# Kernel optimization log

Hardware: AMD Instinct MI355X
Metric: run time of the kernel (lower is better)

Reference implementation:

```python
import jax, jax.numpy as jnp
import numpy as np

N = 100000      # nodes
E = 3200000     # edges
F_IN = 256      # in_channels
H = 64          # hidden_channels
C = 2           # out_channels
G = 128         # graphs in batch


def setup_inputs() -> dict:
    key = jax.random.key(0)
    ks = jax.random.split(key, 10)
    x = jax.random.normal(ks[0], (N, F_IN), jnp.float32)
    edge_index = jax.random.randint(ks[1], (2, E), 0, N, dtype=jnp.int64)
    batch = jnp.sort(jax.random.randint(ks[2], (N,), 0, G, dtype=jnp.int64))
    s = 0.05
    W1 = jax.random.normal(ks[3], (F_IN, H), jnp.float32) * s
    b1 = jnp.zeros((H,), jnp.float32)
    W2 = jax.random.normal(ks[4], (H, H), jnp.float32) * s
    b2 = jnp.zeros((H,), jnp.float32)
    fc_W = jax.random.normal(ks[5], (H, C), jnp.float32) * s
    fc_b = jnp.zeros((C,), jnp.float32)
    return {"x": x, "edge_index": edge_index, "batch": batch,
            "W1": W1, "b1": b1, "W2": W2, "b2": b2,
            "fc_W": fc_W, "fc_b": fc_b}


def _gcn_layer(h, src, dst, norm, W, b, n_nodes):
    # PyG GCNConv: linear transform first, then normalized aggregate, then bias
    h = h @ W                                   # [N, H]
    msg = h[src] * norm[:, None]                # [E+N, H] gather + scale
    out = jax.ops.segment_sum(msg, dst, num_segments=n_nodes)
    return out + b


def reference(x, edge_index, batch, W1, b1, W2, b2, fc_W, fc_b):
    n_nodes = x.shape[0]
    # add self loops (GCNConv default)
    loop = jnp.arange(n_nodes, dtype=edge_index.dtype)
    src = jnp.concatenate([edge_index[0], loop])
    dst = jnp.concatenate([edge_index[1], loop])
    # symmetric normalization D^{-1/2} (A+I) D^{-1/2}
    deg = jax.ops.segment_sum(jnp.ones_like(src, dtype=x.dtype), dst,
                              num_segments=n_nodes)
    deg_isqrt = jnp.where(deg > 0, jax.lax.rsqrt(deg), 0.0)
    norm = deg_isqrt[src] * deg_isqrt[dst]

    h = jax.nn.relu(_gcn_layer(x, src, dst, norm, W1, b1, n_nodes))
    h = jax.nn.relu(_gcn_layer(h, src, dst, norm, W2, b2, n_nodes))

    # global mean pool over graphs
    n_graphs = G
    sums = jax.ops.segment_sum(h, batch, num_segments=n_graphs)
    cnts = jax.ops.segment_sum(jnp.ones((n_nodes,), h.dtype), batch,
                               num_segments=n_graphs)
    pooled = sums / jnp.clip(cnts, 1.0)[:, None]  # [G, H]
    return pooled @ fc_W + fc_b                   # [G, C]
```

## Files before the change

kernel.cpp:

```cpp
#include <hip/hip_runtime.h>
#include <hip/hip_bf16.h>


#define F_IN 256
#define HDIM 64
#define BR_SHIFT 7
#define BRANGE 128
#define BCAP 4608
#define CHUNK 8192
#define NBK 788

typedef short short8 __attribute__((ext_vector_type(8)));
typedef short short4v __attribute__((ext_vector_type(4)));
typedef float float4v __attribute__((ext_vector_type(4)));
typedef _Float16 half_t;

__device__ __forceinline__ unsigned bf16_rn(float f) {
  unsigned u = __builtin_bit_cast(unsigned, f);
  return (u + 0x7FFFu + ((u >> 16) & 1u)) >> 16;
}
__device__ __forceinline__ float bf16_to_f32(unsigned h) {
  return __builtin_bit_cast(float, h << 16);
}

__global__ __launch_bounds__(256) void bin_kernel(
    const int* __restrict__ src, const int* __restrict__ dst,
    int* __restrict__ gcur, int* __restrict__ entries, int E, int nb) {
  __shared__ int out32[CHUNK];
  __shared__ int pref[NBK + 1];
  __shared__ int cur[NBK];
  __shared__ int gbase[NBK];
  __shared__ int sscan[256];
  const int tid = threadIdx.x;
  for (int i = tid; i < nb; i += 256) cur[i] = 0;
  __syncthreads();
  long e0 = (long)blockIdx.x * CHUNK;
  int cnt = (int)min((long)CHUNK, (long)E - e0);
  for (int i = tid; i < cnt; i += 256)
    atomicAdd(&cur[dst[e0 + i] >> BR_SHIFT], 1);
  __syncthreads();
  int b0 = tid * 4;
  int h[4];
  int s = 0;
#pragma unroll
  for (int i = 0; i < 4; ++i) {
    h[i] = (b0 + i < nb) ? cur[b0 + i] : 0;
    s += h[i];
  }
  int x = s;
  sscan[tid] = x;
  __syncthreads();
  for (int off = 1; off < 256; off <<= 1) {
    int t = (tid >= off) ? sscan[tid - off] : 0;
    __syncthreads();
    sscan[tid] += t;
    __syncthreads();
  }
  int run = sscan[tid] - x;
#pragma unroll
  for (int i = 0; i < 4; ++i) {
    if (b0 + i < nb) {
      pref[b0 + i] = run;
      cur[b0 + i] = run;
      if (h[i] > 0) gbase[b0 + i] = atomicAdd(&gcur[b0 + i], h[i]);
      run += h[i];
    }
  }
  if (tid == 0) pref[nb] = cnt;
  __syncthreads();
  for (int i = tid; i < cnt; i += 256) {
    int d = dst[e0 + i];
    int sv = src[e0 + i];
    int b = d >> BR_SHIFT;
    int r = atomicAdd(&cur[b], 1);
    out32[r] = ((d & (BRANGE - 1)) << 17) | sv;
  }
  __syncthreads();
  for (int j = tid; j < cnt; j += 256) {
    int lo = 0, hi = nb - 1;
    while (lo < hi) {
      int mid = (lo + hi + 1) >> 1;
      if (pref[mid] <= j) lo = mid; else hi = mid - 1;
    }
    int b = lo;
    int slot = gbase[b] + (j - pref[b]);
    if (slot < BCAP) entries[(size_t)b * BCAP + slot] = out32[j];
  }
}

__global__ __launch_bounds__(256) void bucket_scan_kernel(
    const int* __restrict__ gcur, int* __restrict__ bbase,
    int* __restrict__ rowptr, int nb, int N, int E) {
  __shared__ int sscan[256];
  const int tid = threadIdx.x;
  int b0 = tid * 4;
  int h[4];
  int s = 0;
#pragma unroll
  for (int i = 0; i < 4; ++i) {
    h[i] = (b0 + i < nb) ? min(gcur[b0 + i], BCAP) : 0;
    s += h[i];
  }
  int x = s;
  sscan[tid] = x;
  __syncthreads();
  for (int off = 1; off < 256; off <<= 1) {
    int t = (tid >= off) ? sscan[tid - off] : 0;
    __syncthreads();
    sscan[tid] += t;
    __syncthreads();
  }
  int run = sscan[tid] - x;
#pragma unroll
  for (int i = 0; i < 4; ++i) {
    if (b0 + i < nb) {
      bbase[b0 + i] = run;
      run += h[i];
    }
  }
  if (tid == 0) rowptr[N] = E;
}

__global__ __launch_bounds__(256) void csr_build_kernel(
    const int* __restrict__ entries, const int* __restrict__ gcur,
    const int* __restrict__ bbase, int* __restrict__ rowptr,
    float* __restrict__ dnorm, int* __restrict__ csr, int N) {
  __shared__ int lbuf[BCAP];
  __shared__ int lcnt[BRANGE];
  __shared__ int lpref[BRANGE];
  __shared__ int lcur[BRANGE];
  const int b = blockIdx.x, tid = threadIdx.x;
  const int v0 = b * BRANGE;
  const int nloc = min(BRANGE, N - v0);
  if (tid < BRANGE) lcnt[tid] = 0;
  __syncthreads();
  const int cnt = min(gcur[b], BCAP);
  const int base = bbase[b];
  const int* ep = entries + (size_t)b * BCAP;
  for (int i = tid; i < cnt; i += 256) atomicAdd(&lcnt[ep[i] >> 17], 1);
  __syncthreads();
  if (tid < BRANGE) lpref[tid] = lcnt[tid];
  __syncthreads();
  for (int off = 1; off < BRANGE; off <<= 1) {
    int t = 0;
    if (tid < BRANGE && tid >= off) t = lpref[tid - off];
    __syncthreads();
    if (tid < BRANGE) lpref[tid] += t;
    __syncthreads();
  }
  if (tid < BRANGE) {
    int excl = lpref[tid] - lcnt[tid];
    lcur[tid] = excl;
    if (tid < nloc) {
      rowptr[v0 + tid] = base + excl;
      dnorm[v0 + tid] = rsqrtf((float)lcnt[tid] + 1.0f);
    }
  }
  __syncthreads();
  for (int i = tid; i < cnt; i += 256) {
    int e = ep[i];
    int dl = e >> 17;
    int pos = atomicAdd(&lcur[dl], 1);
    if (pos < BCAP) lbuf[pos] = e & 0x1FFFF;
  }
  __syncthreads();
  int* outp = csr + base;
  for (int i = tid; i < cnt; i += 256) outp[i] = lbuf[i];
}

template <int K>
__global__ __launch_bounds__(256) void wfrag_kernel(
    const float* __restrict__ W, short* __restrict__ whi,
    short* __restrict__ wlo) {
  constexpr int KS = K / 32;
  int slot = blockIdx.x * 256 + threadIdx.x;
  if (slot >= 4 * KS * 64 * 8) return;
  int j = slot & 7;
  int lane = (slot >> 3) & 63;
  int fk = slot >> 9;
  int ks = fk % KS;
  int ct = fk / KS;
  int k = ks * 32 + (lane >> 4) * 8 + j;
  int n = ct * 16 + (lane & 15);
  float w = W[k * 64 + n];
  unsigned h = bf16_rn(w);
  unsigned l = bf16_rn(w - bf16_to_f32(h));
  whi[slot] = (short)h;
  wlo[slot] = (short)l;
}

template <int K, typename OT>
__global__ __launch_bounds__(512) void mfma_gemm_kernel(
    const float* __restrict__ X, const short* __restrict__ whi,
    const short* __restrict__ wlo, const float* __restrict__ dnorm,
    OT* __restrict__ out, int N) {
  constexpr int KS = K / 32;
  constexpr int P = K + 8;
  __shared__ __align__(16) short Ahi[64 * P];
  __shared__ __align__(16) short Alo[64 * P];
  const int tid = threadIdx.x;
  const long base = (long)blockIdx.x * 64;
  constexpr int C4 = K / 4;
  constexpr int NL = 64 * C4 / 512;
#pragma unroll
  for (int i = 0; i < NL; ++i) {
    int idx = tid + i * 512;
    int row = idx / C4;
    int c4 = idx % C4;
    long r = base + row;
    if (r >= N) r = N - 1;
    float4v v = *(const float4v*)&X[(size_t)r * K + c4 * 4];
    short4v hv, lv;
#pragma unroll
    for (int j = 0; j < 4; ++j) {
      float f = v[j];
      unsigned h = bf16_rn(f);
      unsigned l = bf16_rn(f - bf16_to_f32(h));
      hv[j] = (short)h;
      lv[j] = (short)l;
    }
    *(short4v*)&Ahi[row * P + c4 * 4] = hv;
    *(short4v*)&Alo[row * P + c4 * 4] = lv;
  }
  __syncthreads();
  const int lane = tid & 63;
  const int wave = tid >> 6;
  const int rt = wave & 3;
  const int chalf = wave >> 2;
  const int m = lane & 15;
  const int q = lane >> 4;
  const int arow = rt * 16 + m;
  float4v acc[2];
  acc[0] = (float4v){0.f, 0.f, 0.f, 0.f};
  acc[1] = (float4v){0.f, 0.f, 0.f, 0.f};
  for (int ks = 0; ks < KS; ++ks) {
    int koff = ks * 32 + q * 8;
    short8 ah = *(const short8*)&Ahi[arow * P + koff];
    short8 al = *(const short8*)&Alo[arow * P + koff];
#pragma unroll
    for (int cc = 0; cc < 2; ++cc) {
      int ct = chalf * 2 + cc;
      size_t fo = ((size_t)(ct * KS + ks) * 64 + lane) * 8;
      short8 bh = *(const short8*)&whi[fo];
      short8 bl = *(const short8*)&wlo[fo];
      acc[cc] = __builtin_amdgcn_mfma_f32_16x16x32_bf16(ah, bh, acc[cc], 0, 0, 0);
      acc[cc] = __builtin_amdgcn_mfma_f32_16x16x32_bf16(ah, bl, acc[cc], 0, 0, 0);
      acc[cc] = __builtin_amdgcn_mfma_f32_16x16x32_bf16(al, bh, acc[cc], 0, 0, 0);
    }
  }
#pragma unroll
  for (int reg = 0; reg < 4; ++reg) {
    long grow = base + rt * 16 + q * 4 + reg;
    if (grow < N) {
      float dn = dnorm[grow];
#pragma unroll
      for (int cc = 0; cc < 2; ++cc) {
        int ct = chalf * 2 + cc;
        out[grow * 64 + ct * 16 + m] = (OT)(acc[cc][reg] * dn);
      }
    }
  }
}

__global__ __launch_bounds__(256) void gather_agg_kernel(
    const half_t* __restrict__ hs, const int* __restrict__ rowptr,
    const int* __restrict__ csr, const float* __restrict__ dnorm,
    const float* __restrict__ bias, float* __restrict__ hout, int N) {
  const int lane = threadIdx.x & 63;
  const int wave = __builtin_amdgcn_readfirstlane((int)(threadIdx.x >> 6));
  int v = blockIdx.x * 4 + wave;
  if (v >= N) return;
  int beg = rowptr[v], end = rowptr[v + 1];
  float a0 = (float)hs[(size_t)v * 64 + lane];
  float a1 = 0.f, a2 = 0.f, a3 = 0.f, a4 = 0.f, a5 = 0.f, a6 = 0.f, a7 = 0.f;
  int j = beg;
  for (; j + 8 <= end; j += 8) {
    int s0 = csr[j], s1 = csr[j + 1], s2 = csr[j + 2], s3 = csr[j + 3];
    int s4 = csr[j + 4], s5 = csr[j + 5], s6 = csr[j + 6], s7 = csr[j + 7];
    a0 += (float)hs[(size_t)s0 * 64 + lane];
    a1 += (float)hs[(size_t)s1 * 64 + lane];
    a2 += (float)hs[(size_t)s2 * 64 + lane];
    a3 += (float)hs[(size_t)s3 * 64 + lane];
    a4 += (float)hs[(size_t)s4 * 64 + lane];
    a5 += (float)hs[(size_t)s5 * 64 + lane];
    a6 += (float)hs[(size_t)s6 * 64 + lane];
    a7 += (float)hs[(size_t)s7 * 64 + lane];
  }
  for (; j + 4 <= end; j += 4) {
    int s0 = csr[j], s1 = csr[j + 1], s2 = csr[j + 2], s3 = csr[j + 3];
    a0 += (float)hs[(size_t)s0 * 64 + lane];
    a1 += (float)hs[(size_t)s1 * 64 + lane];
    a2 += (float)hs[(size_t)s2 * 64 + lane];
    a3 += (float)hs[(size_t)s3 * 64 + lane];
  }
  for (; j < end; ++j) a0 += (float)hs[(size_t)csr[j] * 64 + lane];
  float val = dnorm[v] * (((a0 + a1) + (a2 + a3)) + ((a4 + a5) + (a6 + a7))) +
              bias[lane];
  hout[(size_t)v * 64 + lane] = fmaxf(val, 0.f);
}

__global__ __launch_bounds__(256) void gather_agg_pool_kernel(
    const half_t* __restrict__ hs, const int* __restrict__ rowptr,
    const int* __restrict__ csr, const float* __restrict__ dnorm,
    const float* __restrict__ bias, const int* __restrict__ batch,
    float* __restrict__ pooled, int N) {
  const int lane = threadIdx.x & 63;
  const int wave = __builtin_amdgcn_readfirstlane((int)(threadIdx.x >> 6));
  int v = blockIdx.x * 4 + wave;
  if (v >= N) return;
  int beg = rowptr[v], end = rowptr[v + 1];
  float a0 = (float)hs[(size_t)v * 64 + lane];
  float a1 = 0.f, a2 = 0.f, a3 = 0.f, a4 = 0.f, a5 = 0.f, a6 = 0.f, a7 = 0.f;
  int j = beg;
  for (; j + 8 <= end; j += 8) {
    int s0 = csr[j], s1 = csr[j + 1], s2 = csr[j + 2], s3 = csr[j + 3];
    int s4 = csr[j + 4], s5 = csr[j + 5], s6 = csr[j + 6], s7 = csr[j + 7];
    a0 += (float)hs[(size_t)s0 * 64 + lane];
    a1 += (float)hs[(size_t)s1 * 64 + lane];
    a2 += (float)hs[(size_t)s2 * 64 + lane];
    a3 += (float)hs[(size_t)s3 * 64 + lane];
    a4 += (float)hs[(size_t)s4 * 64 + lane];
    a5 += (float)hs[(size_t)s5 * 64 + lane];
    a6 += (float)hs[(size_t)s6 * 64 + lane];
    a7 += (float)hs[(size_t)s7 * 64 + lane];
  }
  for (; j + 4 <= end; j += 4) {
    int s0 = csr[j], s1 = csr[j + 1], s2 = csr[j + 2], s3 = csr[j + 3];
    a0 += (float)hs[(size_t)s0 * 64 + lane];
    a1 += (float)hs[(size_t)s1 * 64 + lane];
    a2 += (float)hs[(size_t)s2 * 64 + lane];
    a3 += (float)hs[(size_t)s3 * 64 + lane];
  }
  for (; j < end; ++j) a0 += (float)hs[(size_t)csr[j] * 64 + lane];
  float val = dnorm[v] * (((a0 + a1) + (a2 + a3)) + ((a4 + a5) + (a6 + a7))) +
              bias[lane];
  val = fmaxf(val, 0.f);
  atomicAdd(&pooled[(size_t)batch[v] * 64 + lane], val);
}

__global__ __launch_bounds__(256) void final_fc_kernel(
    const float* __restrict__ pooled, const int* __restrict__ batch,
    const float* __restrict__ fcW, const float* __restrict__ fcb,
    float* __restrict__ out, int G, int N) {
  int t = blockIdx.x * 256 + threadIdx.x;
  if (t < G * 2) {
    int g = t >> 1, c = t & 1;
    int lo = 0, hi = N;
    while (lo < hi) { int m = (lo + hi) >> 1; if (batch[m] < g) lo = m + 1; else hi = m; }
    int lb = lo;
    lo = 0; hi = N;
    while (lo < hi) { int m = (lo + hi) >> 1; if (batch[m] <= g) lo = m + 1; else hi = m; }
    int cntg = lo - lb;
    float inv = 1.0f / fmaxf((float)cntg, 1.0f);
    float acc = fcb[c];
#pragma unroll
    for (int h = 0; h < 64; ++h)
      acc = fmaf(pooled[g * 64 + h] * inv, fcW[h * 2 + c], acc);
    out[t] = acc;
  }
}

extern "C" void kernel_launch(void* const* d_in, const int* in_sizes, int n_in,
                              void* d_out, int out_size, void* d_ws, size_t ws_size,
                              hipStream_t stream) {
  const float* x   = (const float*)d_in[0];
  const int*   ei  = (const int*)d_in[1];
  const int*   bat = (const int*)d_in[2];
  const float* W1  = (const float*)d_in[3];
  const float* b1  = (const float*)d_in[4];
  const float* W2  = (const float*)d_in[5];
  const float* b2  = (const float*)d_in[6];
  const float* fcW = (const float*)d_in[7];
  const float* fcb = (const float*)d_in[8];
  float* out = (float*)d_out;

  const int N = in_sizes[0] / F_IN;
  const int E = in_sizes[1] / 2;
  const int G = out_size / 2;
  const int* src = ei;
  const int* dst = ei + E;
  const int nb  = (N + BRANGE - 1) >> BR_SHIFT;

  auto aln = [](size_t v) { return (v + 63) & ~(size_t)63; };
  char* w = (char*)d_ws;
  int*    entries = (int*)w;     w += aln((size_t)nb * BCAP * 4);
  int*    gcur    = (int*)w;     w += aln((size_t)nb * 4);
  int*    bbase   = (int*)w;     w += aln((size_t)nb * 4);
  int*    rowptr  = (int*)w;     w += aln((size_t)(N + 1) * 4);
  float*  dnorm   = (float*)w;   w += aln((size_t)N * 4);
  int*    csr     = (int*)w;     w += aln((size_t)E * 4);
  half_t* hs      = (half_t*)w;  w += aln((size_t)N * 64 * 2);
  float*  h1      = (float*)w;   w += aln((size_t)N * 64 * 4);
  float*  pooled  = (float*)w;   w += aln((size_t)G * 64 * 4);
  short*  whi1    = (short*)w;   w += aln((size_t)F_IN * 64 * 2);
  short*  wlo1    = (short*)w;   w += aln((size_t)F_IN * 64 * 2);
  short*  whi2    = (short*)w;   w += aln((size_t)HDIM * 64 * 2);
  short*  wlo2    = (short*)w;   w += aln((size_t)HDIM * 64 * 2);

  hipMemsetAsync(gcur, 0, (size_t)nb * 4, stream);
  hipMemsetAsync(pooled, 0, (size_t)G * 64 * 4, stream);

  wfrag_kernel<F_IN><<<(F_IN * 64 * 8 / 8 + 255) / 256, 256, 0, stream>>>(W1, whi1, wlo1);
  wfrag_kernel<HDIM><<<(HDIM * 64 * 8 / 8 + 255) / 256, 256, 0, stream>>>(W2, whi2, wlo2);

  bin_kernel<<<(E + CHUNK - 1) / CHUNK, 256, 0, stream>>>(
      src, dst, gcur, entries, E, nb);
  bucket_scan_kernel<<<1, 256, 0, stream>>>(gcur, bbase, rowptr, nb, N, E);
  csr_build_kernel<<<nb, 256, 0, stream>>>(entries, gcur, bbase, rowptr,
                                           dnorm, csr, N);

  mfma_gemm_kernel<F_IN, half_t><<<(N + 63) / 64, 512, 0, stream>>>(
      x, whi1, wlo1, dnorm, hs, N);
  gather_agg_kernel<<<(N + 3) / 4, 256, 0, stream>>>(hs, rowptr, csr, dnorm, b1, h1, N);

  mfma_gemm_kernel<HDIM, half_t><<<(N + 63) / 64, 512, 0, stream>>>(
      h1, whi2, wlo2, dnorm, hs, N);
  gather_agg_pool_kernel<<<(N + 3) / 4, 256, 0, stream>>>(hs, rowptr, csr, dnorm, b2, bat, pooled, N);

  final_fc_kernel<<<1, 256, 0, stream>>>(pooled, bat, fcW, fcb, out, G, N);
}
```

Measured before the change: 538.5 us.

## Gather four neighbors per wave with 8-byte half4 loads and shuffle reduction

Restructures the aggregation kernels so each wave splits into four 16-lane groups, each group loading a different neighbor row as 8-byte half4 vectors. Partial sums are combined with cross-group shuffles. This cuts the number of load instructions per edge and raises memory-level parallelism. The tail is handled with masked loads that may read up to 32 csr entries past the row end, so the csr buffer is padded by 64 entries. Pool atomics are issued by one group per wave, with four atomics per lane.

```diff
diff --git a/kernel.cpp b/kernel.cpp
--- a/kernel.cpp
+++ b/kernel.cpp
@@ -14,6 +14,7 @@
 typedef short short4v __attribute__((ext_vector_type(4)));
 typedef float float4v __attribute__((ext_vector_type(4)));
 typedef _Float16 half_t;
+typedef _Float16 half4v __attribute__((ext_vector_type(4)));
 
 __device__ __forceinline__ unsigned bf16_rn(float f) {
   unsigned u = __builtin_bit_cast(unsigned, f);
@@ -262,41 +263,100 @@
   }
 }
 
+__device__ __forceinline__ float4v gather_sum(
+    const half_t* __restrict__ hs, const int* __restrict__ csr,
+    int beg, int end, int v, int g, int q) {
+  float4v a0 = {0.f, 0.f, 0.f, 0.f};
+  float4v a1 = a0, a2 = a0, a3 = a0;
+  const size_t co = (size_t)(q << 2);
+  int j = beg;
+
+#define GCN_SEL(u)                                                         \
+    int t0 = csr[j + 4 * (u)], t1 = csr[j + 4 * (u) + 1],                  \
+        t2 = csr[j + 4 * (u) + 2], t3 = csr[j + 4 * (u) + 3];              \
+    int idx = g == 0 ? t0 : (g == 1 ? t1 : (g == 2 ? t2 : t3));
+
+  for (; j + 32 <= end; j += 32) {
+    half4v h0, h1, h2, h3, h4, h5, h6, h7;
+    { GCN_SEL(0) h0 = *(const half4v*)&hs[((size_t)idx << 6) + co]; }
+    { GCN_SEL(1) h1 = *(const half4v*)&hs[((size_t)idx << 6) + co]; }
+    { GCN_SEL(2) h2 = *(const half4v*)&hs[((size_t)idx << 6) + co]; }
+    { GCN_SEL(3) h3 = *(const half4v*)&hs[((size_t)idx << 6) + co]; }
+    { GCN_SEL(4) h4 = *(const half4v*)&hs[((size_t)idx << 6) + co]; }
+    { GCN_SEL(5) h5 = *(const half4v*)&hs[((size_t)idx << 6) + co]; }
+    { GCN_SEL(6) h6 = *(const half4v*)&hs[((size_t)idx << 6) + co]; }
+    { GCN_SEL(7) h7 = *(const half4v*)&hs[((size_t)idx << 6) + co]; }
+#pragma unroll
+    for (int k = 0; k < 4; ++k) {
+      a0[k] += (float)h0[k]; a1[k] += (float)h1[k];
+      a2[k] += (float)h2[k]; a3[k] += (float)h3[k];
+      a0[k] += (float)h4[k]; a1[k] += (float)h5[k];
+      a2[k] += (float)h6[k]; a3[k] += (float)h7[k];
+    }
+  }
+  if (j < end) {
+    const int r = end - j;
+    half4v h0, h1, h2, h3, h4, h5, h6, h7;
+    float s0, s1, s2, s3, s4, s5, s6, s7;
+#define GCN_MSEL(u, H, S)                                                  \
+    { GCN_SEL(u)                                                           \
+      bool p = (4 * (u) + g) < r;                                          \
+      idx = p ? idx : v;                                                   \
+      S = p ? 1.0f : 0.0f;                                                 \
+      H = *(const half4v*)&hs[((size_t)idx << 6) + co]; }
+    GCN_MSEL(0, h0, s0)
+    GCN_MSEL(1, h1, s1)
+    GCN_MSEL(2, h2, s2)
+    GCN_MSEL(3, h3, s3)
+    GCN_MSEL(4, h4, s4)
+    GCN_MSEL(5, h5, s5)
+    GCN_MSEL(6, h6, s6)
+    GCN_MSEL(7, h7, s7)
+#pragma unroll
+    for (int k = 0; k < 4; ++k) {
+      a0[k] = fmaf((float)h0[k], s0, a0[k]);
+      a1[k] = fmaf((float)h1[k], s1, a1[k]);
+      a2[k] = fmaf((float)h2[k], s2, a2[k]);
+      a3[k] = fmaf((float)h3[k], s3, a3[k]);
+      a0[k] = fmaf((float)h4[k], s4, a0[k]);
+      a1[k] = fmaf((float)h5[k], s5, a1[k]);
+      a2[k] = fmaf((float)h6[k], s6, a2[k]);
+      a3[k] = fmaf((float)h7[k], s7, a3[k]);
+    }
+#undef GCN_MSEL
+  }
+#undef GCN_SEL
+  float4v t = (a0 + a1) + (a2 + a3);
+#pragma unroll
+  for (int k = 0; k < 4; ++k) {
+    float x = t[k];
+    x += __shfl_xor(x, 16);
+    x += __shfl_xor(x, 32);
+    t[k] = x;
+  }
+  return t;
+}
+
 __global__ __launch_bounds__(256) void gather_agg_kernel(
     const half_t* __restrict__ hs, const int* __restrict__ rowptr,
     const int* __restrict__ csr, const float* __restrict__ dnorm,
     const float* __restrict__ bias, float* __restrict__ hout, int N) {
   const int lane = threadIdx.x & 63;
   const int wave = __builtin_amdgcn_readfirstlane((int)(threadIdx.x >> 6));
+  const int g = lane >> 4;
+  const int q = lane & 15;
   int v = blockIdx.x * 4 + wave;
   if (v >= N) return;
   int beg = rowptr[v], end = rowptr[v + 1];
-  float a0 = (float)hs[(size_t)v * 64 + lane];
-  float a1 = 0.f, a2 = 0.f, a3 = 0.f, a4 = 0.f, a5 = 0.f, a6 = 0.f, a7 = 0.f;
-  int j = beg;
-  for (; j + 8 <= end; j += 8) {
-    int s0 = csr[j], s1 = csr[j + 1], s2 = csr[j + 2], s3 = csr[j + 3];
-    int s4 = csr[j + 4], s5 = csr[j + 5], s6 = csr[j + 6], s7 = csr[j + 7];
-    a0 += (float)hs[(size_t)s0 * 64 + lane];
-    a1 += (float)hs[(size_t)s1 * 64 + lane];
-    a2 += (float)hs[(size_t)s2 * 64 + lane];
-    a3 += (float)hs[(size_t)s3 * 64 + lane];
-    a4 += (float)hs[(size_t)s4 * 64 + lane];
-    a5 += (float)hs[(size_t)s5 * 64 + lane];
-    a6 += (float)hs[(size_t)s6 * 64 + lane];
-    a7 += (float)hs[(size_t)s7 * 64 + lane];
-  }
-  for (; j + 4 <= end; j += 4) {
-    int s0 = csr[j], s1 = csr[j + 1], s2 = csr[j + 2], s3 = csr[j + 3];
-    a0 += (float)hs[(size_t)s0 * 64 + lane];
-    a1 += (float)hs[(size_t)s1 * 64 + lane];
-    a2 += (float)hs[(size_t)s2 * 64 + lane];
-    a3 += (float)hs[(size_t)s3 * 64 + lane];
-  }
-  for (; j < end; ++j) a0 += (float)hs[(size_t)csr[j] * 64 + lane];
-  float val = dnorm[v] * (((a0 + a1) + (a2 + a3)) + ((a4 + a5) + (a6 + a7))) +
-              bias[lane];
-  hout[(size_t)v * 64 + lane] = fmaxf(val, 0.f);
+  float4v t = gather_sum(hs, csr, beg, end, v, g, q);
+  half4v sv = *(const half4v*)&hs[((size_t)v << 6) + (q << 2)];
+  float dn = dnorm[v];
+  float4v b4 = *(const float4v*)&bias[q << 2];
+  float4v o;
+#pragma unroll
+  for (int k = 0; k < 4; ++k)
+    o[k] = fmaxf(dn * (t[k] + (float)sv[k]) + b4[k], 0.f);
+  if (g == 0) *(float4v*)&hout[((size_t)v << 6) + (q << 2)] = o;
 }
 
 __global__ __launch_bounds__(256) void gather_agg_pool_kernel(
@@ -306,36 +366,27 @@
     float* __restrict__ pooled, int N) {
   const int lane = threadIdx.x & 63;
   const int wave = __builtin_amdgcn_readfirstlane((int)(threadIdx.x >> 6));
+  const int g = lane >> 4;
+  const int q = lane & 15;
   int v = blockIdx.x * 4 + wave;
   if (v >= N) return;
   int beg = rowptr[v], end = rowptr[v + 1];
-  float a0 = (float)hs[(size_t)v * 64 + lane];
-  float a1 = 0.f, a2 = 0.f, a3 = 0.f, a4 = 0.f, a5 = 0.f, a6 = 0.f, a7 = 0.f;
-  int j = beg;
-  for (; j + 8 <= end; j += 8) {
-    int s0 = csr[j], s1 = csr[j + 1], s2 = csr[j + 2], s3 = csr[j + 3];
-    int s4 = csr[j + 4], s5 = csr[j + 5], s6 = csr[j + 6], s7 = csr[j + 7];
-    a0 += (float)hs[(size_t)s0 * 64 + lane];
-    a1 += (float)hs[(size_t)s1 * 64 + lane];
-    a2 += (float)hs[(size_t)s2 * 64 + lane];
-    a3 += (float)hs[(size_t)s3 * 64 + lane];
-    a4 += (float)hs[(size_t)s4 * 64 + lane];
-    a5 += (float)hs[(size_t)s5 * 64 + lane];
-    a6 += (float)hs[(size_t)s6 * 64 + lane];
-    a7 += (float)hs[(size_t)s7 * 64 + lane];
-  }
-  for (; j + 4 <= end; j += 4) {
-    int s0 = csr[j], s1 = csr[j + 1], s2 = csr[j + 2], s3 = csr[j + 3];
-    a0 += (float)hs[(size_t)s0 * 64 + lane];
-    a1 += (float)hs[(size_t)s1 * 64 + lane];
-    a2 += (float)hs[(size_t)s2 * 64 + lane];
-    a3 += (float)hs[(size_t)s3 * 64 + lane];
-  }
-  for (; j < end; ++j) a0 += (float)hs[(size_t)csr[j] * 64 + lane];
-  float val = dnorm[v] * (((a0 + a1) + (a2 + a3)) + ((a4 + a5) + (a6 + a7))) +
-              bias[lane];
-  val = fmaxf(val, 0.f);
-  atomicAdd(&pooled[(size_t)batch[v] * 64 + lane], val);
+  float4v t = gather_sum(hs, csr, beg, end, v, g, q);
+  half4v sv = *(const half4v*)&hs[((size_t)v << 6) + (q << 2)];
+  float dn = dnorm[v];
+  float4v b4 = *(const float4v*)&bias[q << 2];
+  float4v o;
+#pragma unroll
+  for (int k = 0; k < 4; ++k)
+    o[k] = fmaxf(dn * (t[k] + (float)sv[k]) + b4[k], 0.f);
+  if (g == 0) {
+    int b = batch[v];
+    float* pb = &pooled[((size_t)b << 6) + (q << 2)];
+    atomicAdd(pb + 0, o[0]);
+    atomicAdd(pb + 1, o[1]);
+    atomicAdd(pb + 2, o[2]);
+    atomicAdd(pb + 3, o[3]);
+  }
 }
 
 __global__ __launch_bounds__(256) void final_fc_kernel(
@@ -388,7 +439,7 @@
   int*    bbase   = (int*)w;     w += aln((size_t)nb * 4);
   int*    rowptr  = (int*)w;     w += aln((size_t)(N + 1) * 4);
   float*  dnorm   = (float*)w;   w += aln((size_t)N * 4);
-  int*    csr     = (int*)w;     w += aln((size_t)E * 4);
+  int*    csr     = (int*)w;     w += aln((size_t)(E + 64) * 4);
   half_t* hs      = (half_t*)w;  w += aln((size_t)N * 64 * 2);
   float*  h1      = (float*)w;   w += aln((size_t)N * 64 * 4);
   float*  pooled  = (float*)w;   w += aln((size_t)G * 64 * 4);
```

Result: slower. 776.3 us (+44.2%).
